# Optimization experiments

Measured on AMD Instinct MI355X. Metric: run time of the kernel, lower is better.

Reference implementation:

```python
import jax, jax.numpy as jnp
import numpy as np
from jax import lax

HID = 128  # hidden_dim
K = 2      # kernel (must be 2 for the torch slice arithmetic to be shape-consistent)


def skew(x):
    # x: (B,C,H,W) -> (B,C,H,2W-1), row r shifted right by r
    B, C, H, W = x.shape
    rows = jnp.arange(H)[:, None]
    cols = jnp.arange(W)[None, :] + rows
    y = jnp.zeros((B, C, H, 2 * W - 1), x.dtype)
    return y.at[:, :, rows, cols].set(x)


def unskew(x):
    B, C, H, Wp = x.shape
    W = (Wp + 1) // 2
    rows = jnp.arange(H)[:, None]
    cols = jnp.arange(W)[None, :] + rows
    return x[:, :, rows, cols]


def setup_inputs() -> dict:
    key = jax.random.key(0)
    k1, k2, k3 = jax.random.split(key, 3)
    Cin = 128
    x = jax.random.normal(k1, (8, Cin, 64, 64), jnp.float32)
    w_is = jax.random.normal(k2, (4 * HID, Cin), jnp.float32) * 0.05   # 1x1 conv weight
    b_is = jnp.zeros((4 * HID,), jnp.float32)
    w_ss = jax.random.normal(k3, (4 * HID, HID, K, 1), jnp.float32) * 0.05  # (k,1) conv weight
    b_ss = jnp.zeros((4 * HID,), jnp.float32)
    return {"x": x, "w_is": w_is, "b_is": b_is, "w_ss": w_ss, "b_ss": b_ss}


def reference(x, w_is, b_is, w_ss, b_ss):
    B, Cin, H, W = x.shape
    hid, k = HID, K
    xs = skew(x)  # (B,Cin,H,2W-1)
    # input-to-state: 1x1 conv (mask B on 1x1 kernel == plain 1x1 conv)
    z_is = jnp.einsum('bchw,oc->bohw', xs, w_is) + b_is[None, :, None, None]
    steps = z_is.transpose(3, 0, 1, 2)  # (2W-1, B, 4hid, H)

    h0 = jnp.zeros((B, hid, H), x.dtype)
    c0 = jnp.zeros((B, hid, H), x.dtype)

    def step(carry, z_t):
        h, c = carry  # (B,hid,H)
        # state-to-state (k,1) conv along H, padding k//2, then drop last k-1 rows
        hs = lax.conv_general_dilated(h[..., None], w_ss, (1, 1),
                                      [(k // 2, k // 2), (0, 0)],
                                      dimension_numbers=('NCHW', 'OIHW', 'NCHW'))
        hs = hs[:, :, :-(k - 1), 0] + b_ss[None, :, None]  # (B,4hid,H)
        z = z_t + hs
        i = jax.nn.sigmoid(z[:, :hid])
        f = jax.nn.sigmoid(z[:, hid:2 * hid])
        o = jax.nn.sigmoid(z[:, 2 * hid:3 * hid])
        g = jnp.tanh(z[:, 3 * hid:])
        c = f * c + i * g
        h = o * jnp.tanh(c)
        return (h, c), h

    _, hs_all = lax.scan(step, (h0, c0), steps)  # (2W-1,B,hid,H)
    out = hs_all.transpose(1, 2, 3, 0)  # (B,hid,H,2W-1)
    return unskew(out)  # (B,hid,H,W)
```

## Files before the change

kernel.cpp:

```cpp
#include <hip/hip_runtime.h>
#include <hip/hip_fp16.h>
#include <math.h>


#define HID 128
#define BB 8
#define HH 64
#define WW 64
#define TT 127

#define NPREP 1024

#define NZPRE 224

#define HROW 136

typedef _Float16 v8h __attribute__((ext_vector_type(8)));
typedef float v4f __attribute__((ext_vector_type(4)));

#define SENT64 0xFFFFFFFFFFFFFFFFULL

__device__ __forceinline__ float fsig(float x) {
  float e = __builtin_amdgcn_exp2f(x * -1.44269504f);
  return __builtin_amdgcn_rcpf(1.f + e);
}
__device__ __forceinline__ float ftanh_(float x) {
  float e = __builtin_amdgcn_exp2f(x * 2.88539009f);
  return __builtin_fmaf(-2.f, __builtin_amdgcn_rcpf(1.f + e), 1.f);
}

__global__ __launch_bounds__(256) void prep_k(
    const float* __restrict__ w_ss, const float* __restrict__ b_is,
    const float* __restrict__ b_ss, _Float16* __restrict__ wp,
    __half* __restrict__ zph, unsigned* __restrict__ zflag,
    unsigned long long* __restrict__ hx) {
  int idx = blockIdx.x * 256 + threadIdx.x;
  if (idx < 131072) {
    int j = idx & 7;
    int L = (idx >> 3) & 63;
    int kt = (idx >> 9) & 7;
    int mt = idx >> 12;
    int O = mt * 16 + (L & 15);
    int k = kt * 32 + ((L >> 4) & 3) * 8 + j;
    float v = (k < 128) ? w_ss[(size_t)O * 256 + k * 2]
                        : w_ss[(size_t)O * 256 + (k - 128) * 2 + 1];
    wp[idx] = (_Float16)v;
  } else if (idx < 131584) {
    int idx2 = idx - 131072;
    int g = (idx2 >> 2) & 3;
    int u = (idx2 >> 4) * 4 + (idx2 & 3);
    int O = g * 128 + u;
    zph[(size_t)BB * HH * WW * 512 + idx2] = __float2half(b_is[O] + b_ss[O]);
  } else if (idx < 132096) {
    zflag[idx - 131584] = 0u;
  } else {
    int j = idx - 132096;
    uint4 s;
    s.x = 0xFFFFFFFFu; s.y = 0xFFFFFFFFu;
    s.z = 0xFFFFFFFFu; s.w = 0xFFFFFFFFu;
    ((uint4*)hx)[j] = s;
  }
}

#define STEP_BARRIER()                                   \
  do {                                                   \
    asm volatile("s_waitcnt lgkmcnt(0)" ::: "memory");   \
    __builtin_amdgcn_s_barrier();                        \
    asm volatile("" ::: "memory");                       \
  } while (0)

#define HPLD(p) __hip_atomic_load((p), __ATOMIC_RELAXED, __HIP_MEMORY_SCOPE_AGENT)

#define STEP_BODY(T, RB)                                                       \
  do {                                                                         \
           \
    v8h bfr[4];                                                                \
    _Pragma("unroll") for (int kt = 0; kt < 4; kt++)                           \
        bfr[kt] = *(const v8h*)&h_lds[RB][(rl * 2 + bl) * HROW + kt * 32 +     \
                                          quad * 8];                           \
                               \
    v4f zi[4];                                                                 \
    _Pragma("unroll") for (int g = 0; g < 4; g++)                              \
        _Pragma("unroll") for (int i = 0; i < 4; i++)                          \
        zi[g][i] = __half2float(zu.h[g * 4 + i]);                              \
        \
    {                                                                          \
      if (!zdone && (unsigned)wn < WW) {                                       \
        while (__hip_atomic_load(zf, __ATOMIC_RELAXED,                         \
                                 __HIP_MEMORY_SCOPE_AGENT) == 0u)              \
          __builtin_amdgcn_s_sleep(2);                                         \
        __builtin_amdgcn_fence(__ATOMIC_ACQUIRE, "agent");                     \
        zdone = true;                                                          \
      }                                                                        \
      const uint4* p = (const uint4*)(((unsigned)wn < WW) ? zcur : zbias);     \
      zu.q[0] = p[0];                                                          \
      zu.q[1] = p[1];                                                          \
      wn++;                                                                    \
      zcur += 512;                                                             \
    }                                                                          \
          \
    v4f acc0[4], acc1[4];                                                      \
    _Pragma("unroll") for (int g = 0; g < 4; g++) {                            \
      acc0[g] = (v4f){0.f, 0.f, 0.f, 0.f};                                     \
      acc1[g] = zi[g];                                                         \
    }                                                                          \
    _Pragma("unroll") for (int kt = 0; kt < 4; kt++) {                         \
      _Pragma("unroll") for (int g = 0; g < 4; g++)                            \
          acc0[g] = __builtin_amdgcn_mfma_f32_16x16x32_f16(                    \
              wfrag[g][kt], bfr[kt], acc0[g], 0, 0, 0);                        \
    }                                                                          \
    _Pragma("unroll") for (int kt = 0; kt < 4; kt++) {                         \
      v8h bf1 = *(const v8h*)&h_lds[RB][((rl + 1) * 2 + bl) * HROW + kt * 32 + \
                                        quad * 8];                             \
      _Pragma("unroll") for (int g = 0; g < 4; g++)                            \
          acc1[g] = __builtin_amdgcn_mfma_f32_16x16x32_f16(                    \
              wfrag[g][4 + kt], bf1, acc1[g], 0, 0, 0);                        \
    }                                                                          \
         \
    unsigned long long pend = 0ull;                                            \
    if (is_cons) pend = HPLD(ca);                                              \
                        \
    const int w = (T)-r;                                                       \
    const bool inband = ((unsigned)w < WW);                                    \
    float hv[4];                                                               \
    _Pragma("unroll") for (int rg2 = 0; rg2 < 4; rg2++) {                      \
      float z0 = acc0[0][rg2] + acc1[0][rg2];                                  \
      float z1 = acc0[1][rg2] + acc1[1][rg2];                                  \
      float z2 = acc0[2][rg2] + acc1[2][rg2];                                  \
      float z3 = acc0[3][rg2] + acc1[3][rg2];                                  \
      float iv = fsig(z0);                                                     \
      float fv = fsig(z1);                                                     \
      float ov = fsig(z2);                                                     \
      float gv = ftanh_(z3);                                                   \
      c[rg2] = fv * c[rg2] + iv * gv;                                          \
      hv[rg2] = ov * ftanh_(c[rg2]);                                           \
    }                                                                          \
                       \
    __half2 plo = __floats2half2_rn(hv[0], hv[1]);                             \
    __half2 phi = __floats2half2_rn(hv[2], hv[3]);                             \
    {                                                                          \
      uint2 pk;                                                                \
      pk.x = *(unsigned*)&plo;                                                 \
      pk.y = *(unsigned*)&phi;                                                 \
      *(uint2*)&h_lds[(RB) ^ 1][((rl + 1) * 2 + bl) * HROW + uq0] = pk;        \
    }                                                                          \
              \
    if (rgr < 7 && l15 >= 14) {                                                \
      unsigned long long pk =                                                  \
          ((unsigned long long)*(unsigned*)&phi << 32) | *(unsigned*)&plo;     \
      __hip_atomic_store(pa_hx, pk, __ATOMIC_RELAXED,                          \
                         __HIP_MEMORY_SCOPE_AGENT);                            \
    }                                                                          \
    pa_hx += 2048;                                                             \
             \
    _Pragma("unroll") for (int rg2 = 0; rg2 < 4; rg2++) {                      \
      outb[rg2].x = outb[rg2].y;                                               \
      outb[rg2].y = outb[rg2].z;                                               \
      outb[rg2].z = outb[rg2].w;                                               \
      outb[rg2].w = hv[rg2];                                                   \
    }                                                                          \
    if (inband && (w & 3) == 3) {                                              \
      *(float4*)op0 = outb[0];                                                 \
      *(float4*)op1 = outb[1];                                                 \
      *(float4*)op2 = outb[2];                                                 \
      *(float4*)op3 = outb[3];                                                 \
      op0 += 4; op1 += 4; op2 += 4; op3 += 4;                                  \
    }                                                                          \
                          \
    if (is_cons) {                                                             \
      while (__ballot(pend == SENT64) != 0ull) {                               \
        __builtin_amdgcn_s_sleep(1);                                           \
        pend = HPLD(ca);                                                       \
      }                                                                        \
      *(unsigned long long*)&h_lds[(RB) ^ 1][(0 * 2 + ebl) * HROW + eu] =      \
          pend;                                                                \
    }                                                                          \
    ca += 2048;                                                                \
    STEP_BARRIER();                                                            \
  } while (0)

__global__ __launch_bounds__(512, 1) void fused(
    const __half* __restrict__ zph, const _Float16* __restrict__ wp,
    unsigned long long* __restrict__ hx, float* __restrict__ out,
    const float* __restrict__ x, const float* __restrict__ w_is,
    const float* __restrict__ b_is, const float* __restrict__ b_ss,
    unsigned* __restrict__ zflag, __half* __restrict__ zphw) {
  __shared__ _Float16 h_lds[2][9 * 2 * HROW];
  __shared__ _Float16 xt[64][136];

  const int blk = blockIdx.x;
  const int tid = threadIdx.x;
  const int L = tid & 63;
  const int quad = L >> 4;
  const int l15 = L & 15;

  if (blk >= 32) {
    const int j = blk - 32;
    const int wv8 = tid >> 6;

    v8h wfr[4][4];
    float4 bvv[4];
#pragma unroll
    for (int m = 0; m < 4; m++) {
      const int mt = 4 * wv8 + m;
      const int O = mt * 16 + l15;
#pragma unroll
      for (int kt = 0; kt < 4; kt++) {
        const float* p = w_is + (size_t)O * 128 + kt * 32 + quad * 8;
        float4 a = *(const float4*)p;
        float4 b2 = *(const float4*)(p + 4);
        v8h f;
        f[0] = (_Float16)a.x;  f[1] = (_Float16)a.y;
        f[2] = (_Float16)a.z;  f[3] = (_Float16)a.w;
        f[4] = (_Float16)b2.x; f[5] = (_Float16)b2.y;
        f[6] = (_Float16)b2.z; f[7] = (_Float16)b2.w;
        wfr[m][kt] = f;
      }
      const int O4 = mt * 16 + quad * 4;
      float4 bi = *(const float4*)&b_is[O4];
      float4 bs4 = *(const float4*)&b_ss[O4];
      bvv[m] = make_float4(bi.x + bs4.x, bi.y + bs4.y, bi.z + bs4.z,
                           bi.w + bs4.w);
    }

    for (int tt = j; tt < 512; tt += NZPRE) {
      const int r = tt >> 3;
      const int b = tt & 7;

      __syncthreads();
      {
        const int cw = tid >> 4;
        const int w4 = (tid & 15) * 4;
#pragma unroll
        for (int p = 0; p < 4; p++) {
          int cc = p * 32 + cw;
          float4 v =
              *(const float4*)&x[(((size_t)b * 128 + cc) * HH + r) * WW + w4];
          xt[w4 + 0][cc] = (_Float16)v.x;
          xt[w4 + 1][cc] = (_Float16)v.y;
          xt[w4 + 2][cc] = (_Float16)v.z;
          xt[w4 + 3][cc] = (_Float16)v.w;
        }
      }
      __syncthreads();

#pragma unroll
      for (int nt = 0; nt < 4; nt++) {
        v8h bf[4];
#pragma unroll
        for (int kt = 0; kt < 4; kt++)
          bf[kt] = *(const v8h*)&xt[nt * 16 + l15][kt * 32 + quad * 8];
        const size_t pos = ((size_t)b * HH + r) * WW + nt * 16 + l15;
#pragma unroll
        for (int m = 0; m < 4; m++) {
          v4f acc = (v4f){0.f, 0.f, 0.f, 0.f};
#pragma unroll
          for (int kt = 0; kt < 4; kt++)
            acc = __builtin_amdgcn_mfma_f32_16x16x32_f16(wfr[m][kt], bf[kt],
                                                         acc, 0, 0, 0);
          const int mt = 4 * wv8 + m;
          __half2 lo = __floats2half2_rn(acc[0] + bvv[m].x, acc[1] + bvv[m].y);
          __half2 hi = __floats2half2_rn(acc[2] + bvv[m].z, acc[3] + bvv[m].w);
          uint2 pk;
          pk.x = *(unsigned*)&lo;
          pk.y = *(unsigned*)&hi;
          *(uint2*)&zphw[pos * 512 + ((mt & 7) * 4 + quad) * 16 +
                         (mt >> 3) * 4] = pk;
        }
      }

      __syncthreads();
      if (tid == 0) {
        __builtin_amdgcn_fence(__ATOMIC_RELEASE, "agent");
        __hip_atomic_store(&zflag[tt], 1u, __ATOMIC_RELAXED,
                           __HIP_MEMORY_SCOPE_AGENT);
      }
    }
    return;
  }

  __builtin_amdgcn_s_setprio(1);

  const int rgr = blk >> 2;
  const int bg = blk & 3;
  const int R0 = rgr * 8;
  const int wv = tid >> 6;
  const int rl = l15 >> 1;
  const int bl = l15 & 1;
  const int b = bg * 2 + bl;
  const int r = R0 + rl;
  const int uq0 = 16 * wv + quad * 4;
  const int zoff = (4 * wv + quad) * 16;

  for (int i = tid; i < (2 * 9 * 2 * HROW) / 2; i += 512)
    ((unsigned*)h_lds)[i] = 0u;

  v8h wfrag[4][8];
  {
    const v8h* wp8 = (const v8h*)wp;
#pragma unroll
    for (int g = 0; g < 4; g++)
#pragma unroll
      for (int kt = 0; kt < 8; kt++)
        wfrag[g][kt] = wp8[((size_t)((8 * g + wv) * 8 + kt)) * 64 + L];
  }

  float c[4] = {0.f, 0.f, 0.f, 0.f};
  float4 outb[4];
#pragma unroll
  for (int i = 0; i < 4; i++) outb[i] = make_float4(0.f, 0.f, 0.f, 0.f);

  const int ebl = L >> 5;
  const int eu = (L & 31) * 4;
  const int exp_idx = bl * 32 + 4 * wv + quad;

  const bool is_cons = (wv == 0) && (rgr > 0);

  const __half* zpp = zph + ((size_t)b * HH + r) * WW * 512 + zoff;
  const __half* zbias = zph + (size_t)BB * HH * WW * 512 + zoff;
  const unsigned long long* ca =
      hx + (((size_t)(rgr > 0 ? rgr - 1 : 0) * 4 + bg) * 64 + L);
  unsigned long long* pa_hx = hx + (((size_t)rgr * 4 + bg) * 64 + exp_idx);
  float* op0 = out + (((size_t)b * HID + uq0 + 0) * HH + r) * WW;
  float* op1 = out + (((size_t)b * HID + uq0 + 1) * HH + r) * WW;
  float* op2 = out + (((size_t)b * HID + uq0 + 2) * HH + r) * WW;
  float* op3 = out + (((size_t)b * HID + uq0 + 3) * HH + r) * WW;

  unsigned* zf = &zflag[r * 8 + b];
  bool zdone = false;

  union ZU {
    uint4 q[2];
    __half h[16];
  } zu;
  {
    if (r == 0) {
      while (__hip_atomic_load(zf, __ATOMIC_RELAXED,
                               __HIP_MEMORY_SCOPE_AGENT) == 0u)
        __builtin_amdgcn_s_sleep(2);
      __builtin_amdgcn_fence(__ATOMIC_ACQUIRE, "agent");
      zdone = true;
    }
    const uint4* p0 = (const uint4*)((r == 0) ? zpp : zbias);
    zu.q[0] = p0[0];
    zu.q[1] = p0[1];
  }
  int wn = 1 - r;
  const __half* zcur = zpp + (ptrdiff_t)wn * 512;

  __syncthreads();

  for (int t = 0; t < TT - 1; t += 2) {
    STEP_BODY(t, 0);
    STEP_BODY(t + 1, 1);
  }
  STEP_BODY(TT - 1, 0);
}

__global__ __launch_bounds__(256) void transpose_x(const float* __restrict__ x,
                                                   float* __restrict__ xT) {
  int b = blockIdx.x >> 6;
  int r = blockIdx.x & 63;
  __shared__ float tile[32][65];
  for (int cc = 0; cc < 4; cc++) {
    int cl = threadIdx.x >> 6;
    int w = threadIdx.x & 63;
#pragma unroll
    for (int k = 0; k < 8; k++) {
      int c_loc = k * 4 + cl;
      int c = cc * 32 + c_loc;
      tile[c_loc][w] = x[(((size_t)b * 128 + c) * HH + r) * WW + w];
    }
    __syncthreads();
    int cs = threadIdx.x & 31;
    int wp = threadIdx.x >> 5;
#pragma unroll
    for (int k = 0; k < 8; k++) {
      int w2 = wp * 8 + k;
      xT[(((size_t)b * HH + r) * WW + w2) * 128 + cc * 32 + cs] = tile[cs][w2];
    }
    __syncthreads();
  }
}

__global__ __launch_bounds__(256) void step_kernel(
    const float* __restrict__ x, const float* __restrict__ xT, int use_xT,
    const float* __restrict__ w_is, const float* __restrict__ b_is,
    const float* __restrict__ w_ss, const float* __restrict__ b_ss,
    const float* __restrict__ h_prev, float* __restrict__ h_next,
    float* __restrict__ c_state, float* __restrict__ out, int t) {
  const int rg = blockIdx.x;
  const int q = blockIdx.y;
  const int r0 = rg * 2;
  const int tid = threadIdx.x;
  const int o_loc = tid & 63;
  const int k4 = tid >> 6;
  const int g_ = o_loc >> 4;
  const int u_ = o_loc & 15;
  const int O = g_ * 128 + q * 16 + u_;
  const int i0 = k4 * 32;

  __shared__ __align__(16) float h_in[3][BB][HID];
  __shared__ float zred[16][4][65];

  for (int idx = tid; idx < 3 * BB * HID; idx += 256) {
    int row_sel = idx >> 10;
    int rem = idx & 1023;
    int b = rem >> 7;
    int u = rem & 127;
    int rr = r0 - 1 + row_sel;
    h_in[row_sel][b][u] = (rr >= 0) ? h_prev[((size_t)b * HH + rr) * HID + u] : 0.0f;
  }

  float wr0[32], wr1[32], wz[32];
  {
    const float4* wss4 = (const float4*)(w_ss + ((size_t)O * 128 + i0) * 2);
#pragma unroll
    for (int j = 0; j < 16; j++) {
      float4 v = wss4[j];
      wr0[2 * j] = v.x;
      wr1[2 * j] = v.y;
      wr0[2 * j + 1] = v.z;
      wr1[2 * j + 1] = v.w;
    }
    const float4* wis4 = (const float4*)(w_is + (size_t)O * 128 + i0);
#pragma unroll
    for (int j = 0; j < 8; j++) {
      float4 v = wis4[j];
      wz[4 * j] = v.x;
      wz[4 * j + 1] = v.y;
      wz[4 * j + 2] = v.z;
      wz[4 * j + 3] = v.w;
    }
  }

  __syncthreads();

  float acc[2][BB];
#pragma unroll
  for (int rl = 0; rl < 2; rl++)
#pragma unroll
    for (int b = 0; b < BB; b++) acc[rl][b] = 0.0f;

#pragma unroll
  for (int jb = 0; jb < 8; jb++) {
    int ib = i0 + jb * 4;
#pragma unroll
    for (int b = 0; b < BB; b++) {
      const float4 hm4 = *(const float4*)&h_in[0][b][ib];
      const float4 hc4 = *(const float4*)&h_in[1][b][ib];
      const float4 hp4 = *(const float4*)&h_in[2][b][ib];
      const float* hm = (const float*)&hm4;
      const float* hc = (const float*)&hc4;
      const float* hq = (const float*)&hp4;
#pragma unroll
      for (int jj = 0; jj < 4; jj++) {
        float w0v = wr0[jb * 4 + jj];
        float w1v = wr1[jb * 4 + jj];
        acc[0][b] += w0v * hm[jj] + w1v * hc[jj];
        acc[1][b] += w0v * hc[jj] + w1v * hq[jj];
      }
    }
  }

#pragma unroll
  for (int rl = 0; rl < 2; rl++) {
    int rr = r0 + rl;
    int wcol = t - rr;
    if (wcol >= 0 && wcol < WW) {
      if (use_xT) {
        for (int b = 0; b < BB; b++) {
          const float4* xp =
              (const float4*)(xT + (((size_t)b * HH + rr) * WW + wcol) * 128 + i0);
#pragma unroll
          for (int j = 0; j < 8; j++) {
            float4 v = xp[j];
            acc[rl][b] += wz[4 * j] * v.x + wz[4 * j + 1] * v.y +
                          wz[4 * j + 2] * v.z + wz[4 * j + 3] * v.w;
          }
        }
      } else {
        for (int b = 0; b < BB; b++) {
          const float* xb = x + (((size_t)b * 128 + i0) * HH + rr) * WW + wcol;
#pragma unroll
          for (int j = 0; j < 32; j++) {
            acc[rl][b] += wz[j] * xb[(size_t)j * HH * WW];
          }
        }
      }
    }
  }

#pragma unroll
  for (int rl = 0; rl < 2; rl++)
#pragma unroll
    for (int b = 0; b < BB; b++) zred[rl * 8 + b][k4][o_loc] = acc[rl][b];
  __syncthreads();

  {
    int u = tid >> 4;
    int cell = tid & 15;
    int rl = cell >> 3;
    int b = cell & 7;
    int rr = r0 + rl;
    float z[4];
#pragma unroll
    for (int gg = 0; gg < 4; gg++) {
      int ol = gg * 16 + u;
      float s = zred[cell][0][ol] + zred[cell][1][ol] + zred[cell][2][ol] +
                zred[cell][3][ol];
      int Og = gg * 128 + q * 16 + u;
      z[gg] = s + b_is[Og] + b_ss[Og];
    }
    float iv = 1.0f / (1.0f + expf(-z[0]));
    float fv = 1.0f / (1.0f + expf(-z[1]));
    float ov = 1.0f / (1.0f + expf(-z[2]));
    float gv = tanhf(z[3]);
    int U = q * 16 + u;
    size_t sidx = ((size_t)b * HH + rr) * HID + U;
    float cv = c_state[sidx];
    float cn = fv * cv + iv * gv;
    c_state[sidx] = cn;
    float hn = ov * tanhf(cn);
    h_next[sidx] = hn;
    int wcol = t - rr;
    if (wcol >= 0 && wcol < WW) {
      out[(((size_t)b * HID + U) * HH + rr) * WW + wcol] = hn;
    }
  }
}

extern "C" void kernel_launch(void* const* d_in, const int* in_sizes, int n_in,
                              void* d_out, int out_size, void* d_ws,
                              size_t ws_size, hipStream_t stream) {
  const float* x = (const float*)d_in[0];
  const float* w_is = (const float*)d_in[1];
  const float* b_is = (const float*)d_in[2];
  const float* w_ss = (const float*)d_in[3];
  const float* b_ss = (const float*)d_in[4];
  float* outp = (float*)d_out;

  const size_t zph_bytes = ((size_t)BB * HH * WW * 512 + 512) * 2;
  const size_t wp_bytes = (size_t)512 * 256 * 2;
  const size_t hx_bytes = (size_t)TT * 8 * 4 * 64 * 8;
  const size_t zflag_bytes = 512 * sizeof(unsigned);
  const size_t need = zph_bytes + wp_bytes + hx_bytes + zflag_bytes;

  char* ws = (char*)d_ws;
  if (ws_size >= need) {
    __half* zph = (__half*)ws;
    _Float16* wpp = (_Float16*)(ws + zph_bytes);
    unsigned long long* hx =
        (unsigned long long*)(ws + zph_bytes + wp_bytes);
    unsigned* zflag = (unsigned*)(ws + zph_bytes + wp_bytes + hx_bytes);

    prep_k<<<dim3(NPREP), 256, 0, stream>>>(w_ss, b_is, b_ss, wpp, zph,
                                            zflag, hx);
    fused<<<dim3(32 + NZPRE), 512, 0, stream>>>(zph, wpp, hx, outp, x, w_is,
                                                b_is, b_ss, zflag, zph);
  } else {
    const size_t xT_elems = (size_t)BB * HH * WW * 128;
    const size_t st_elems = (size_t)BB * HH * HID;
    const size_t need_xT = (xT_elems + 3 * st_elems) * sizeof(float);
    float* wsf = (float*)d_ws;
    float* xT = nullptr;
    float* st;
    int use_xT = 0;
    if (ws_size >= need_xT) {
      use_xT = 1;
      xT = wsf;
      st = wsf + xT_elems;
    } else {
      st = wsf;
    }
    float* h0 = st;
    float* h1 = st + st_elems;
    float* cb = st + 2 * st_elems;
    hipMemsetAsync(st, 0, 3 * st_elems * sizeof(float), stream);
    if (use_xT) transpose_x<<<dim3(BB * HH), 256, 0, stream>>>(x, xT);
    for (int t = 0; t < TT; t++) {
      float* hp = (t & 1) ? h1 : h0;
      float* hn = (t & 1) ? h0 : h1;
      step_kernel<<<dim3(32, 8), 256, 0, stream>>>(x, xT, use_xT, w_is, b_is,
                                                   w_ss, b_ss, hp, hn, cb, outp,
                                                   t);
    }
  }
}
```

Measured before the change: 322.5 us.

## Fold prep kernel into fused kernel and stage z-precompute writes through LDS

```diff
diff --git a/kernel.cpp b/kernel.cpp
--- a/kernel.cpp
+++ b/kernel.cpp
@@ -9,11 +9,11 @@
 #define WW 64
 #define TT 127
 
-#define NPREP 1024
-
-#define NZPRE 224
-
+#define NZB 128
 #define HROW 136
+
+#define SMEM_BYTES 50688
+#define XT_BYTES 17408
 
 typedef _Float16 v8h __attribute__((ext_vector_type(8)));
 typedef float v4f __attribute__((ext_vector_type(4)));
@@ -27,39 +27,6 @@
 __device__ __forceinline__ float ftanh_(float x) {
   float e = __builtin_amdgcn_exp2f(x * 2.88539009f);
   return __builtin_fmaf(-2.f, __builtin_amdgcn_rcpf(1.f + e), 1.f);
-}
-
-__global__ __launch_bounds__(256) void prep_k(
-    const float* __restrict__ w_ss, const float* __restrict__ b_is,
-    const float* __restrict__ b_ss, _Float16* __restrict__ wp,
-    __half* __restrict__ zph, unsigned* __restrict__ zflag,
-    unsigned long long* __restrict__ hx) {
-  int idx = blockIdx.x * 256 + threadIdx.x;
-  if (idx < 131072) {
-    int j = idx & 7;
-    int L = (idx >> 3) & 63;
-    int kt = (idx >> 9) & 7;
-    int mt = idx >> 12;
-    int O = mt * 16 + (L & 15);
-    int k = kt * 32 + ((L >> 4) & 3) * 8 + j;
-    float v = (k < 128) ? w_ss[(size_t)O * 256 + k * 2]
-                        : w_ss[(size_t)O * 256 + (k - 128) * 2 + 1];
-    wp[idx] = (_Float16)v;
-  } else if (idx < 131584) {
-    int idx2 = idx - 131072;
-    int g = (idx2 >> 2) & 3;
-    int u = (idx2 >> 4) * 4 + (idx2 & 3);
-    int O = g * 128 + u;
-    zph[(size_t)BB * HH * WW * 512 + idx2] = __float2half(b_is[O] + b_ss[O]);
-  } else if (idx < 132096) {
-    zflag[idx - 131584] = 0u;
-  } else {
-    int j = idx - 132096;
-    uint4 s;
-    s.x = 0xFFFFFFFFu; s.y = 0xFFFFFFFFu;
-    s.z = 0xFFFFFFFFu; s.w = 0xFFFFFFFFu;
-    ((uint4*)hx)[j] = s;
-  }
 }
 
 #define STEP_BARRIER()                                   \
@@ -180,13 +147,12 @@
   } while (0)
 
 __global__ __launch_bounds__(512, 1) void fused(
-    const __half* __restrict__ zph, const _Float16* __restrict__ wp,
-    unsigned long long* __restrict__ hx, float* __restrict__ out,
-    const float* __restrict__ x, const float* __restrict__ w_is,
+    const __half* __restrict__ zph, unsigned long long* __restrict__ hx,
+    float* __restrict__ out, const float* __restrict__ x,
+    const float* __restrict__ w_is, const float* __restrict__ w_ss,
     const float* __restrict__ b_is, const float* __restrict__ b_ss,
     unsigned* __restrict__ zflag, __half* __restrict__ zphw) {
-  __shared__ _Float16 h_lds[2][9 * 2 * HROW];
-  __shared__ _Float16 xt[64][136];
+  __shared__ __align__(16) char smem[SMEM_BYTES];
 
   const int blk = blockIdx.x;
   const int tid = threadIdx.x;
@@ -195,6 +161,8 @@
   const int l15 = L & 15;
 
   if (blk >= 32) {
+    _Float16(*xt)[136] = (_Float16(*)[136])smem;
+    _Float16(*zt)[520] = (_Float16(*)[520])(smem + XT_BYTES);
     const int j = blk - 32;
     const int wv8 = tid >> 6;
 
@@ -223,7 +191,8 @@
                            bi.w + bs4.w);
     }
 
-    for (int tt = j; tt < 512; tt += NZPRE) {
+    for (int it = 0; it < 4; it++) {
+      const int tt = j + NZB * it;
       const int r = tt >> 3;
       const int b = tt & 7;
 
@@ -245,31 +214,45 @@
       __syncthreads();
 
 #pragma unroll
-      for (int nt = 0; nt < 4; nt++) {
-        v8h bf[4];
-#pragma unroll
-        for (int kt = 0; kt < 4; kt++)
-          bf[kt] = *(const v8h*)&xt[nt * 16 + l15][kt * 32 + quad * 8];
-        const size_t pos = ((size_t)b * HH + r) * WW + nt * 16 + l15;
-#pragma unroll
-        for (int m = 0; m < 4; m++) {
-          v4f acc = (v4f){0.f, 0.f, 0.f, 0.f};
+      for (int p = 0; p < 2; p++) {
+#pragma unroll
+        for (int ntl = 0; ntl < 2; ntl++) {
+          const int nt = 2 * p + ntl;
+          v8h bf[4];
 #pragma unroll
           for (int kt = 0; kt < 4; kt++)
-            acc = __builtin_amdgcn_mfma_f32_16x16x32_f16(wfr[m][kt], bf[kt],
-                                                         acc, 0, 0, 0);
-          const int mt = 4 * wv8 + m;
-          __half2 lo = __floats2half2_rn(acc[0] + bvv[m].x, acc[1] + bvv[m].y);
-          __half2 hi = __floats2half2_rn(acc[2] + bvv[m].z, acc[3] + bvv[m].w);
-          uint2 pk;
-          pk.x = *(unsigned*)&lo;
-          pk.y = *(unsigned*)&hi;
-          *(uint2*)&zphw[pos * 512 + ((mt & 7) * 4 + quad) * 16 +
-                         (mt >> 3) * 4] = pk;
+            bf[kt] = *(const v8h*)&xt[nt * 16 + l15][kt * 32 + quad * 8];
+#pragma unroll
+          for (int m = 0; m < 4; m++) {
+            v4f acc = (v4f){0.f, 0.f, 0.f, 0.f};
+#pragma unroll
+            for (int kt = 0; kt < 4; kt++)
+              acc = __builtin_amdgcn_mfma_f32_16x16x32_f16(wfr[m][kt], bf[kt],
+                                                           acc, 0, 0, 0);
+            const int mt = 4 * wv8 + m;
+            __half2 lo =
+                __floats2half2_rn(acc[0] + bvv[m].x, acc[1] + bvv[m].y);
+            __half2 hi =
+                __floats2half2_rn(acc[2] + bvv[m].z, acc[3] + bvv[m].w);
+            uint2 pk;
+            pk.x = *(unsigned*)&lo;
+            pk.y = *(unsigned*)&hi;
+            *(uint2*)&zt[ntl * 16 + l15][((mt & 7) * 4 + quad) * 16 +
+                                         (mt >> 3) * 4] = pk;
+          }
         }
+        __syncthreads();
+        const size_t gbase = ((((size_t)b * HH + r) * WW) + p * 32) * 512;
+#pragma unroll
+        for (int k2 = 0; k2 < 4; k2++) {
+          int u = tid + k2 * 512;
+          int oh = u * 8;
+          uint4 v = *(const uint4*)&zt[oh >> 9][oh & 511];
+          *(uint4*)&zphw[gbase + oh] = v;
+        }
+        __syncthreads();
       }
 
-      __syncthreads();
       if (tid == 0) {
         __builtin_amdgcn_fence(__ATOMIC_RELEASE, "agent");
         __hip_atomic_store(&zflag[tt], 1u, __ATOMIC_RELAXED,
@@ -280,6 +263,7 @@
   }
 
   __builtin_amdgcn_s_setprio(1);
+  _Float16(*h_lds)[9 * 2 * HROW] = (_Float16(*)[9 * 2 * HROW])smem;
 
   const int rgr = blk >> 2;
   const int bg = blk & 3;
@@ -293,17 +277,40 @@
   const int zoff = (4 * wv + quad) * 16;
 
   for (int i = tid; i < (2 * 9 * 2 * HROW) / 2; i += 512)
-    ((unsigned*)h_lds)[i] = 0u;
+    ((unsigned*)smem)[i] = 0u;
+
+  {
+    int g = (tid >> 2) & 3;
+    int u2 = (tid >> 4) * 4 + (tid & 3);
+    int O = g * 128 + u2;
+    zphw[(size_t)BB * HH * WW * 512 + blk * 512 + tid] =
+        __float2half(b_is[O] + b_ss[O]);
+  }
 
   v8h wfrag[4][8];
-  {
-    const v8h* wp8 = (const v8h*)wp;
-#pragma unroll
-    for (int g = 0; g < 4; g++)
-#pragma unroll
-      for (int kt = 0; kt < 8; kt++)
-        wfrag[g][kt] = wp8[((size_t)((8 * g + wv) * 8 + kt)) * 64 + L];
-  }
+#pragma unroll
+  for (int g = 0; g < 4; g++) {
+    const float* wb = w_ss + (size_t)((8 * g + wv) * 16 + l15) * 256;
+#pragma unroll
+    for (int kt2 = 0; kt2 < 4; kt2++) {
+      const float4* p4 = (const float4*)(wb + kt2 * 64 + quad * 16);
+      float4 f0 = p4[0], f1 = p4[1], f2 = p4[2], f3 = p4[3];
+      v8h e, o;
+      e[0] = (_Float16)f0.x; e[1] = (_Float16)f0.z;
+      e[2] = (_Float16)f1.x; e[3] = (_Float16)f1.z;
+      e[4] = (_Float16)f2.x; e[5] = (_Float16)f2.z;
+      e[6] = (_Float16)f3.x; e[7] = (_Float16)f3.z;
+      o[0] = (_Float16)f0.y; o[1] = (_Float16)f0.w;
+      o[2] = (_Float16)f1.y; o[3] = (_Float16)f1.w;
+      o[4] = (_Float16)f2.y; o[5] = (_Float16)f2.w;
+      o[6] = (_Float16)f3.y; o[7] = (_Float16)f3.w;
+      wfrag[g][kt2] = e;
+      wfrag[g][kt2 + 4] = o;
+    }
+  }
+
+  asm volatile("s_waitcnt vmcnt(0)" ::: "memory");
+  __syncthreads();
 
   float c[4] = {0.f, 0.f, 0.f, 0.f};
   float4 outb[4];
@@ -317,7 +324,7 @@
   const bool is_cons = (wv == 0) && (rgr > 0);
 
   const __half* zpp = zph + ((size_t)b * HH + r) * WW * 512 + zoff;
-  const __half* zbias = zph + (size_t)BB * HH * WW * 512 + zoff;
+  const __half* zbias = zph + (size_t)BB * HH * WW * 512 + blk * 512 + zoff;
   const unsigned long long* ca =
       hx + (((size_t)(rgr > 0 ? rgr - 1 : 0) * 4 + bg) * 64 + L);
   unsigned long long* pa_hx = hx + (((size_t)rgr * 4 + bg) * 64 + exp_idx);
@@ -540,24 +547,21 @@
   const float* b_ss = (const float*)d_in[4];
   float* outp = (float*)d_out;
 
-  const size_t zph_bytes = ((size_t)BB * HH * WW * 512 + 512) * 2;
-  const size_t wp_bytes = (size_t)512 * 256 * 2;
+  const size_t zph_bytes = ((size_t)BB * HH * WW * 512 + 32 * 512) * 2;
   const size_t hx_bytes = (size_t)TT * 8 * 4 * 64 * 8;
   const size_t zflag_bytes = 512 * sizeof(unsigned);
-  const size_t need = zph_bytes + wp_bytes + hx_bytes + zflag_bytes;
+  const size_t need = zph_bytes + hx_bytes + zflag_bytes;
 
   char* ws = (char*)d_ws;
   if (ws_size >= need) {
     __half* zph = (__half*)ws;
-    _Float16* wpp = (_Float16*)(ws + zph_bytes);
-    unsigned long long* hx =
-        (unsigned long long*)(ws + zph_bytes + wp_bytes);
-    unsigned* zflag = (unsigned*)(ws + zph_bytes + wp_bytes + hx_bytes);
-
-    prep_k<<<dim3(NPREP), 256, 0, stream>>>(w_ss, b_is, b_ss, wpp, zph,
-                                            zflag, hx);
-    fused<<<dim3(32 + NZPRE), 512, 0, stream>>>(zph, wpp, hx, outp, x, w_is,
-                                                b_is, b_ss, zflag, zph);
+    unsigned long long* hx = (unsigned long long*)(ws + zph_bytes);
+    unsigned* zflag = (unsigned*)(ws + zph_bytes + hx_bytes);
+
+    hipMemsetAsync(hx, 0xFF, hx_bytes, stream);
+    hipMemsetAsync(zflag, 0, zflag_bytes, stream);
+    fused<<<dim3(32 + NZB), 512, 0, stream>>>(zph, hx, outp, x, w_is, w_ss,
+                                              b_is, b_ss, zflag, zph);
   } else {
     const size_t xT_elems = (size_t)BB * HH * WW * 128;
     const size_t st_elems = (size_t)BB * HH * HID;
```

Measured after the change: 324.2 us. Within noise of the previous version (+0.5%).
